# Optimization experiments

Measured on AMD Instinct MI355X. Metric: run time of the kernel, lower is better.

Reference implementation:

```python
import jax, jax.numpy as jnp
import numpy as np

GROUP_SIZE = 128  # per-group quantization granularity along infeatures (K)


def setup_inputs() -> dict:
    key = jax.random.key(0)
    k1, k2, k3, k4, k5 = jax.random.split(key, 5)
    B, K, N, G = 32, 4096, 11008, 4096 // GROUP_SIZE
    x = jax.random.normal(k1, (B, K), dtype=jnp.float16)
    # packed int4 weights: 8 nibbles per int32 along K
    qweight = jax.random.randint(k2, (K // 8, N), 0, 2**31 - 1, dtype=jnp.int32)
    # packed int4 zero points: 8 nibbles per int32 along N, one row per group
    qzeros = jax.random.randint(k3, (G, N // 8), 0, 2**31 - 1, dtype=jnp.int32)
    scales = (jax.random.uniform(k4, (G, N), dtype=jnp.float16) * 0.02 + 0.001).astype(jnp.float16)
    bias = (jax.random.normal(k5, (N,), dtype=jnp.float16) * 0.01).astype(jnp.float16)
    return {"x": x, "qweight": qweight, "qzeros": qzeros, "scales": scales, "bias": bias}


def _unpack_int4(packed, axis):
    # packed int32 -> 8 unsigned 4-bit values, expanded along `axis`
    shifts = (jnp.arange(8, dtype=jnp.int32) * 4)
    shape = [1] * (packed.ndim + 1)
    shape[axis + 1] = 8
    vals = (jnp.expand_dims(packed, axis + 1) >> shifts.reshape(shape)) & 0xF
    new_shape = list(packed.shape)
    new_shape[axis] *= 8
    return vals.reshape(new_shape)


def reference(x, qweight, qzeros, scales, bias):
    K = qweight.shape[0] * 8
    N = qweight.shape[1]
    G = scales.shape[0]
    # unpack weights along K: [K, N] int32 in [0, 15]
    q = _unpack_int4(qweight, axis=0)
    # unpack zero points along N: [G, N]
    z = _unpack_int4(qzeros, axis=1)
    # GPTQ dequant: W[k, n] = scales[g(k), n] * (q[k, n] - (z[g(k), n] + 1))
    qg = q.reshape(G, GROUP_SIZE, N)
    W = ((qg - (z + 1)[:, None, :]).astype(jnp.float16) * scales[:, None, :]).reshape(K, N)
    out = jnp.matmul(x, W, preferred_element_type=jnp.float32).astype(jnp.float16)
    return out + bias
```

## Files before the change

### kernel.cpp

```cpp
#include <hip/hip_runtime.h>
#include <hip/hip_bf16.h>


#define M_ROWS 32
#define K_DIM  4096
#define N_DIM  11008
#define GS     128
#define BN     64
#define KSPLIT 8
#define BKR    (K_DIM / KSPLIT)
#define NGRP   (BKR / GS)
#define XSTR   (BKR + 8)

typedef __bf16 bf16x8 __attribute__((ext_vector_type(8)));
typedef float  f32x4  __attribute__((ext_vector_type(4)));

__global__ void zero_out_kernel(float* __restrict__ out) {
    const int i = (blockIdx.x * 256 + threadIdx.x) * 4;
    if (i < M_ROWS * N_DIM) {
        float4 z = {0.f, 0.f, 0.f, 0.f};
        *(float4*)(&out[i]) = z;
    }
}

__global__ __launch_bounds__(256, 4)
void gptq_mfma_kernel(const float* __restrict__ x,
                      const int* __restrict__ qweight,
                      const int* __restrict__ qzeros,
                      const float* __restrict__ scales,
                      const float* __restrict__ bias,
                      float* __restrict__ out)
{
    __shared__ __align__(16) __bf16 xs[M_ROWS * XSTR];

    const int tid  = threadIdx.x;
    const int lane = tid & 63;
    const int wave = tid >> 6;
    const int n0   = blockIdx.x * BN;
    const int kb   = blockIdx.y;
    const int k0   = kb * BKR;

    const int col  = lane & 15;
    const int quad = lane >> 4;

    #pragma unroll
    for (int i = 0; i < 8; ++i) {
        const int v = i * 256 + tid;
        const int r = v >> 6;
        const int c = (v & 63) * 8;
        const float4 f0 = *(const float4*)(&x[r * K_DIM + k0 + c]);
        const float4 f1 = *(const float4*)(&x[r * K_DIM + k0 + c + 4]);
        bf16x8 hv;
        hv[0] = (__bf16)f0.x; hv[1] = (__bf16)f0.y;
        hv[2] = (__bf16)f0.z; hv[3] = (__bf16)f0.w;
        hv[4] = (__bf16)f1.x; hv[5] = (__bf16)f1.y;
        hv[6] = (__bf16)f1.z; hv[7] = (__bf16)f1.w;
        *(bf16x8*)(&xs[r * XSTR + c]) = hv;
    }
    __syncthreads();

    const int n = n0 + wave * 16 + col;
    f32x4 acc0 = {0.f, 0.f, 0.f, 0.f};
    f32x4 acc1 = {0.f, 0.f, 0.f, 0.f};

    #pragma unroll
    for (int gl = 0; gl < NGRP; ++gl) {
        const int g  = kb * NGRP + gl;
        const int zw = qzeros[g * (N_DIM / 8) + (n >> 3)];
        const float sc = scales[g * N_DIM + n];
        const float zs = (float)(((zw >> ((n & 7) * 4)) & 0xF) + 1) * sc;

        #pragma unroll
        for (int ks = 0; ks < 4; ++ks) {
            const int wrow = kb * (BKR / 8) + gl * (GS / 8) + ks * 4 + quad;
            const int w    = qweight[wrow * N_DIM + n];
            bf16x8 bfrag;
            #pragma unroll
            for (int j = 0; j < 8; ++j) {
                const float qf = (float)((w >> (4 * j)) & 0xF);
                bfrag[j] = (__bf16)(qf * sc - zs);
            }
            const int kk = gl * GS + ks * 32 + quad * 8;
            const bf16x8 a0 = *(const bf16x8*)(&xs[col * XSTR + kk]);
            const bf16x8 a1 = *(const bf16x8*)(&xs[(16 + col) * XSTR + kk]);
            acc0 = __builtin_amdgcn_mfma_f32_16x16x32_bf16(a0, bfrag, acc0, 0, 0, 0);
            acc1 = __builtin_amdgcn_mfma_f32_16x16x32_bf16(a1, bfrag, acc1, 0, 0, 0);
        }
    }

    const float bf = (kb == 0) ? bias[n] : 0.f;
    #pragma unroll
    for (int r = 0; r < 4; ++r) {
        const int m = quad * 4 + r;
        atomicAdd(&out[m * N_DIM + n],        acc0[r] + bf);
        atomicAdd(&out[(16 + m) * N_DIM + n], acc1[r] + bf);
    }
}

extern "C" void kernel_launch(void* const* d_in, const int* in_sizes, int n_in,
                              void* d_out, int out_size, void* d_ws, size_t ws_size,
                              hipStream_t stream) {
    const float* x       = (const float*)d_in[0];
    const int*   qweight = (const int*)d_in[1];
    const int*   qzeros  = (const int*)d_in[2];
    const float* scales  = (const float*)d_in[3];
    const float* bias    = (const float*)d_in[4];
    float*       out     = (float*)d_out;

    zero_out_kernel<<<(M_ROWS * N_DIM + 1023) / 1024, 256, 0, stream>>>(out);

    dim3 grid(N_DIM / BN, KSPLIT);
    gptq_mfma_kernel<<<grid, 256, 0, stream>>>(x, qweight, qzeros, scales, bias, out);
}
```

Measured before the change: 90.78 us.

## Prepack x into MFMA fragment layout and replace atomics with split-K reduce

A new kernel converts x to bf16 once, already laid out in the MFMA A-fragment order, so the main kernel reads A fragments straight from global/L2 and drops its per-block LDS staging and barrier. The atomicAdd split-K accumulation and the zeroing kernel are replaced by per-split partial buffers in the workspace plus a separate reduce kernel that sums them and adds the bias. This removes atomic contention and repeated x conversion, at the cost of an extra launch and about 11 MB of partial-sum traffic.

```diff
diff --git a/kernel.cpp b/kernel.cpp
--- a/kernel.cpp
+++ b/kernel.cpp
@@ -10,56 +10,49 @@
 #define KSPLIT 8
 #define BKR    (K_DIM / KSPLIT)
 #define NGRP   (BKR / GS)
-#define XSTR   (BKR + 8)
+#define OUT_ELEMS (M_ROWS * N_DIM)
+
+#define WS_PART_OFF (256 * 1024)
 
 typedef __bf16 bf16x8 __attribute__((ext_vector_type(8)));
 typedef float  f32x4  __attribute__((ext_vector_type(4)));
 
-__global__ void zero_out_kernel(float* __restrict__ out) {
-    const int i = (blockIdx.x * 256 + threadIdx.x) * 4;
-    if (i < M_ROWS * N_DIM) {
-        float4 z = {0.f, 0.f, 0.f, 0.f};
-        *(float4*)(&out[i]) = z;
-    }
+__global__ __launch_bounds__(256)
+void pack_x_kernel(const float* __restrict__ x, __bf16* __restrict__ xp) {
+    const int gt = blockIdx.x * 256 + threadIdx.x;
+    const int c  = gt >> 6;
+    const int l  = gt & 63;
+    const int t  = c & 1;
+    const int b  = c >> 1;
+    const int m  = 16 * t + (l & 15);
+    const int k0 = 32 * b + (l >> 4) * 8;
+    const float4 f0 = *(const float4*)(&x[m * K_DIM + k0]);
+    const float4 f1 = *(const float4*)(&x[m * K_DIM + k0 + 4]);
+    bf16x8 hv;
+    hv[0] = (__bf16)f0.x; hv[1] = (__bf16)f0.y;
+    hv[2] = (__bf16)f0.z; hv[3] = (__bf16)f0.w;
+    hv[4] = (__bf16)f1.x; hv[5] = (__bf16)f1.y;
+    hv[6] = (__bf16)f1.z; hv[7] = (__bf16)f1.w;
+    *(bf16x8*)(&xp[(size_t)gt * 8]) = hv;
 }
 
 __global__ __launch_bounds__(256, 4)
-void gptq_mfma_kernel(const float* __restrict__ x,
+void gptq_mfma_kernel(const __bf16* __restrict__ xp,
                       const int* __restrict__ qweight,
                       const int* __restrict__ qzeros,
                       const float* __restrict__ scales,
-                      const float* __restrict__ bias,
-                      float* __restrict__ out)
+                      float* __restrict__ part)
 {
-    __shared__ __align__(16) __bf16 xs[M_ROWS * XSTR];
-
     const int tid  = threadIdx.x;
     const int lane = tid & 63;
     const int wave = tid >> 6;
     const int n0   = blockIdx.x * BN;
     const int kb   = blockIdx.y;
-    const int k0   = kb * BKR;
 
     const int col  = lane & 15;
     const int quad = lane >> 4;
+    const int n    = n0 + wave * 16 + col;
 
-    #pragma unroll
-    for (int i = 0; i < 8; ++i) {
-        const int v = i * 256 + tid;
-        const int r = v >> 6;
-        const int c = (v & 63) * 8;
-        const float4 f0 = *(const float4*)(&x[r * K_DIM + k0 + c]);
-        const float4 f1 = *(const float4*)(&x[r * K_DIM + k0 + c + 4]);
-        bf16x8 hv;
-        hv[0] = (__bf16)f0.x; hv[1] = (__bf16)f0.y;
-        hv[2] = (__bf16)f0.z; hv[3] = (__bf16)f0.w;
-        hv[4] = (__bf16)f1.x; hv[5] = (__bf16)f1.y;
-        hv[6] = (__bf16)f1.z; hv[7] = (__bf16)f1.w;
-        *(bf16x8*)(&xs[r * XSTR + c]) = hv;
-    }
-    __syncthreads();
-
-    const int n = n0 + wave * 16 + col;
     f32x4 acc0 = {0.f, 0.f, 0.f, 0.f};
     f32x4 acc1 = {0.f, 0.f, 0.f, 0.f};
 
@@ -80,21 +73,41 @@
                 const float qf = (float)((w >> (4 * j)) & 0xF);
                 bfrag[j] = (__bf16)(qf * sc - zs);
             }
-            const int kk = gl * GS + ks * 32 + quad * 8;
-            const bf16x8 a0 = *(const bf16x8*)(&xs[col * XSTR + kk]);
-            const bf16x8 a1 = *(const bf16x8*)(&xs[(16 + col) * XSTR + kk]);
+            const int b = kb * 16 + gl * 4 + ks;
+            const bf16x8 a0 = *(const bf16x8*)(&xp[((b * 2 + 0) * 64 + lane) * 8]);
+            const bf16x8 a1 = *(const bf16x8*)(&xp[((b * 2 + 1) * 64 + lane) * 8]);
             acc0 = __builtin_amdgcn_mfma_f32_16x16x32_bf16(a0, bfrag, acc0, 0, 0, 0);
             acc1 = __builtin_amdgcn_mfma_f32_16x16x32_bf16(a1, bfrag, acc1, 0, 0, 0);
         }
     }
 
-    const float bf = (kb == 0) ? bias[n] : 0.f;
+    float* p = part + (size_t)kb * OUT_ELEMS;
     #pragma unroll
     for (int r = 0; r < 4; ++r) {
         const int m = quad * 4 + r;
-        atomicAdd(&out[m * N_DIM + n],        acc0[r] + bf);
-        atomicAdd(&out[(16 + m) * N_DIM + n], acc1[r] + bf);
+        p[m * N_DIM + n]        = acc0[r];
+        p[(16 + m) * N_DIM + n] = acc1[r];
     }
+}
+
+__global__ __launch_bounds__(256)
+void reduce_kernel(const float* __restrict__ part,
+                   const float* __restrict__ bias,
+                   float* __restrict__ out)
+{
+    const int i    = blockIdx.x * 256 + threadIdx.x;
+    const int base = i * 4;
+    if (base >= OUT_ELEMS) return;
+    const int n = base % N_DIM;
+    f32x4 s = *(const f32x4*)(&part[base]);
+    #pragma unroll
+    for (int kb = 1; kb < KSPLIT; ++kb) {
+        const f32x4 v = *(const f32x4*)(&part[(size_t)kb * OUT_ELEMS + base]);
+        s += v;
+    }
+    const f32x4 bv = *(const f32x4*)(&bias[n]);
+    s += bv;
+    *(f32x4*)(&out[base]) = s;
 }
 
 extern "C" void kernel_launch(void* const* d_in, const int* in_sizes, int n_in,
@@ -107,8 +120,13 @@
     const float* bias    = (const float*)d_in[4];
     float*       out     = (float*)d_out;
 
-    zero_out_kernel<<<(M_ROWS * N_DIM + 1023) / 1024, 256, 0, stream>>>(out);
+    __bf16* xp   = (__bf16*)d_ws;
+    float*  part = (float*)((char*)d_ws + WS_PART_OFF);
+
+    pack_x_kernel<<<64, 256, 0, stream>>>(x, xp);
 
     dim3 grid(N_DIM / BN, KSPLIT);
-    gptq_mfma_kernel<<<grid, 256, 0, stream>>>(x, qweight, qzeros, scales, bias, out);
+    gptq_mfma_kernel<<<grid, 256, 0, stream>>>(xp, qweight, qzeros, scales, part);
+
+    reduce_kernel<<<(OUT_ELEMS / 4 + 255) / 256, 256, 0, stream>>>(part, bias, out);
 }
```

After: 89.19 us. About the same (-1.8%).
